# Kernel optimization log

Measured on AMD Instinct MI355X. Metric: run time of the kernel, lower is better.

The kernel has to match this reference:

```python
import jax, jax.numpy as jnp
import numpy as np

B, T, H = 4, 8192, 512
LN_EPS = 1e-5


def _ln(x, g, b):
    mu = jnp.mean(x, axis=-1, keepdims=True)
    var = jnp.mean((x - mu) ** 2, axis=-1, keepdims=True)
    return (x - mu) * jax.lax.rsqrt(var + LN_EPS) * g + b


def _log_g(x):
    # log of g(x) = x + 0.5 (x >= 0) else sigmoid(x); both branches NaN-safe.
    return jnp.where(x >= 0, jnp.log(jax.nn.relu(x) + 0.5), -jax.nn.softplus(-x))


def _min_gru(x, Wz, bz, Wh, bh):
    # minGRU parallel log-space scan ("Were RNNs All We Needed?" Alg.), h_0 = 0.
    k = x @ Wz + bz                      # [B,T,H] gate pre-activation
    log_z = -jax.nn.softplus(-k)         # log sigmoid(k)
    log_coeffs = -jax.nn.softplus(k)     # log (1 - sigmoid(k))
    log_tilde_h = _log_g(x @ Wh + bh)
    log_h0 = jnp.full((x.shape[0], 1, x.shape[2]), jnp.log(0.5), x.dtype)  # g(0)=0.5
    log_values = jnp.concatenate([log_h0, log_z + log_tilde_h], axis=1)   # [B,T+1,H]
    a_star = jnp.cumsum(jnp.pad(log_coeffs, ((0, 0), (1, 0), (0, 0))), axis=1)
    log_h = a_star + jax.lax.cumlogsumexp(log_values - a_star, axis=1)
    return jnp.exp(log_h)[:, 1:]         # drop h_0 slot -> [B,T,H]


def setup_inputs() -> dict:
    key = jax.random.key(0)
    ks = jax.random.split(key, 5)
    s = 1.0 / np.sqrt(H)
    return {
        "x": jax.random.normal(ks[0], (B, T, H), jnp.float32),
        "ln1_g": jnp.ones((H,), jnp.float32),
        "ln1_b": jnp.zeros((H,), jnp.float32),
        "Wz": jax.random.normal(ks[1], (H, H), jnp.float32) * s,
        "bz": jnp.zeros((H,), jnp.float32),
        "Wh": jax.random.normal(ks[2], (H, H), jnp.float32) * s,
        "bh": jnp.zeros((H,), jnp.float32),
        "ln2_g": jnp.ones((H,), jnp.float32),
        "ln2_b": jnp.zeros((H,), jnp.float32),
        "W1": jax.random.normal(ks[3], (H, H), jnp.float32) * s,
        "b1": jnp.zeros((H,), jnp.float32),
        "W2": jax.random.normal(ks[4], (H, H), jnp.float32) * s,
        "b2": jnp.zeros((H,), jnp.float32),
    }


def reference(x, ln1_g, ln1_b, Wz, bz, Wh, bh, ln2_g, ln2_b, W1, b1, W2, b2):
    # x = x + minGRU(ln_1(x))   (dropout=0 -> identity)
    x = x + _min_gru(_ln(x, ln1_g, ln1_b), Wz, bz, Wh, bh)
    # x = x + FFN(ln_2(x)) ; FFN = Linear -> ReLU -> Linear (hidden->hidden)
    h = jax.nn.relu(_ln(x, ln2_g, ln2_b) @ W1 + b1)
    x = x + (h @ W2 + b2)
    return x
```

## Files before the change

kernel.cpp:

```cpp
#include <hip/hip_runtime.h>

typedef unsigned short u16;
typedef unsigned int u32;
typedef __bf16 bf16x8 __attribute__((ext_vector_type(8)));
typedef float f32x4 __attribute__((ext_vector_type(4)));
typedef u16 u16x8 __attribute__((ext_vector_type(8)));

__device__ __forceinline__ u16 f2bf(float f) {
    union { float f; u32 i; } v; v.f = f;
    u32 x = v.i;
    u32 r = (x + 0x7fffu + ((x >> 16) & 1u)) >> 16;
    return (u16)r;
}
__device__ __forceinline__ float bf2f(u16 u) {
    union { u32 i; float f; } v; v.i = ((u32)u) << 16; return v.f;
}
__device__ __forceinline__ u16 f2h(float f) {
    union { _Float16 h; u16 u; } v; v.h = (_Float16)f; return v.u;
}
__device__ __forceinline__ float h2f(u16 u) {
    union { _Float16 h; u16 u; } v; v.u = u; return (float)v.h;
}

__device__ __forceinline__ void gld16(const void* g, void* l) {
    __builtin_amdgcn_global_load_lds(
        (const __attribute__((address_space(1))) void*)g,
        (__attribute__((address_space(3))) void*)l, 16, 0, 0);
}

__global__ __launch_bounds__(256) void transpose4(
    const float* __restrict__ s0, const float* __restrict__ s1,
    const float* __restrict__ s2, const float* __restrict__ s3,
    u16* __restrict__ d0, u16* __restrict__ d1,
    u16* __restrict__ d2, u16* __restrict__ d3)
{
    int bx = blockIdx.x;
    int mat = bx >> 8;
    int tile = bx & 255;
    int tx = (tile & 15) * 32;
    int ty = (tile >> 4) * 32;
    const float* src = (mat == 0) ? s0 : (mat == 1) ? s1 : (mat == 2) ? s2 : s3;
    u16* dst = (mat == 0) ? d0 : (mat == 1) ? d1 : (mat == 2) ? d2 : d3;

    __shared__ u16 tl[32][33];
    int col = threadIdx.x & 31;
    int r8  = threadIdx.x >> 5;
    #pragma unroll
    for (int k = 0; k < 4; ++k) {
        int rr = r8 + k * 8;
        tl[rr][col] = f2bf(src[(ty + rr) * 512 + tx + col]);
    }
    __syncthreads();
    #pragma unroll
    for (int k = 0; k < 4; ++k) {
        int rr = r8 + k * 8;
        dst[(tx + rr) * 512 + ty + col] = tl[col][rr];
    }
}

__global__ __launch_bounds__(256) void ln_k(
    const float* __restrict__ x, const float* __restrict__ g,
    const float* __restrict__ b, u16* __restrict__ y, int rows)
{
    int gid = blockIdx.x * blockDim.x + threadIdx.x;
    int row = gid >> 6;
    int lane = gid & 63;
    if (row >= rows) return;

    const float* xr = x + (size_t)row * 512 + lane * 8;
    float4 a0 = *(const float4*)xr;
    float4 a1 = *(const float4*)(xr + 4);
    float f[8] = {a0.x, a0.y, a0.z, a0.w, a1.x, a1.y, a1.z, a1.w};
    float s = 0.f, s2 = 0.f;
    #pragma unroll
    for (int e = 0; e < 8; ++e) { s += f[e]; s2 += f[e] * f[e]; }
    #pragma unroll
    for (int o = 32; o > 0; o >>= 1) { s += __shfl_xor(s, o); s2 += __shfl_xor(s2, o); }
    const float inv = 1.0f / 512.0f;
    float mean = s * inv;
    float var  = s2 * inv - mean * mean;
    float rstd = rsqrtf(var + 1e-5f);

    float4 g0 = *(const float4*)(g + lane * 8);
    float4 g1 = *(const float4*)(g + lane * 8 + 4);
    float4 b0 = *(const float4*)(b + lane * 8);
    float4 b1 = *(const float4*)(b + lane * 8 + 4);
    float gg[8] = {g0.x, g0.y, g0.z, g0.w, g1.x, g1.y, g1.z, g1.w};
    float bb[8] = {b0.x, b0.y, b0.z, b0.w, b1.x, b1.y, b1.z, b1.w};
    u16x8 ov;
    #pragma unroll
    for (int e = 0; e < 8; ++e)
        ov[e] = f2bf((f[e] - mean) * rstd * gg[e] + bb[e]);
    *(u16x8*)(y + (size_t)row * 512 + lane * 8) = ov;
}

__global__ __launch_bounds__(256, 2) void gemm_gate(
    const u16* __restrict__ A, const u16* __restrict__ Bt0,
    const u16* __restrict__ Bt1, const float* __restrict__ bias0,
    const float* __restrict__ bias1, u32* __restrict__ cvb,
    float* __restrict__ chCp, float* __restrict__ chVp)
{
    constexpr int Kd = 512, Nd = 512;
    constexpr int BUF = 12288;
    __shared__ __align__(16) u16 smem[2 * BUF];

    int bx = blockIdx.x;
    bx = (bx & 7) * 128 + (bx >> 3);
    int m0 = (bx >> 2) * 128;
    int n0 = (bx & 3) * 128;
    int tid = threadIdx.x;
    int lane = tid & 63;
    int w = tid >> 6;
    int wm = w & 1, wn = w >> 1;
    int l16 = lane & 15;
    int quad = lane >> 4;

    f32x4 acc0[4][4] = {};
    f32x4 acc1[4][4] = {};

    int ch0 = tid, ch1 = tid + 256;
    int row0 = ch0 >> 2, row1 = ch1 >> 2;
    int g0 = (ch0 & 3) ^ ((ch0 >> 3) & 3);
    int g1 = (ch1 & 3) ^ ((ch1 >> 3) & 3);
    const u16* a0p  = A   + (size_t)(m0 + row0) * Kd + g0 * 8;
    const u16* a1p  = A   + (size_t)(m0 + row1) * Kd + g1 * 8;
    const u16* b00p = Bt0 + (size_t)(n0 + row0) * Kd + g0 * 8;
    const u16* b01p = Bt0 + (size_t)(n0 + row1) * Kd + g1 * 8;
    const u16* b10p = Bt1 + (size_t)(n0 + row0) * Kd + g0 * 8;
    const u16* b11p = Bt1 + (size_t)(n0 + row1) * Kd + g1 * 8;

#define STAGE(sl, kt) { \
    int k0_ = (kt) * 32; \
    u16* L_ = smem + (sl) * BUF; \
    gld16(a0p  + k0_, &L_[ch0 * 8]); \
    gld16(a1p  + k0_, &L_[ch1 * 8]); \
    gld16(b00p + k0_, &L_[4096 + ch0 * 8]); \
    gld16(b01p + k0_, &L_[4096 + ch1 * 8]); \
    gld16(b10p + k0_, &L_[8192 + ch0 * 8]); \
    gld16(b11p + k0_, &L_[8192 + ch1 * 8]); }

    STAGE(0, 0);
    __syncthreads();

    for (int kt = 0; kt < Kd / 32; ++kt) {
        int cur = kt & 1;
        if (kt < Kd / 32 - 1) STAGE(cur ^ 1, kt + 1);

        const u16* As  = smem + cur * BUF;
        const u16* Bs0 = As + 4096;
        const u16* Bs1 = As + 8192;
        bf16x8 af[4], bf0[4], bf1[4];
        #pragma unroll
        for (int i = 0; i < 4; ++i) {
            int ra = wm * 64 + i * 16 + l16;
            int rb = wn * 64 + i * 16 + l16;
            int ga = quad ^ ((ra >> 1) & 3);
            int gb = quad ^ ((rb >> 1) & 3);
            af[i]  = *(const bf16x8*)&As [ra * 32 + ga * 8];
            bf0[i] = *(const bf16x8*)&Bs0[rb * 32 + gb * 8];
            bf1[i] = *(const bf16x8*)&Bs1[rb * 32 + gb * 8];
        }
        #pragma unroll
        for (int i = 0; i < 4; ++i)
            #pragma unroll
            for (int j = 0; j < 4; ++j) {
                acc0[i][j] = __builtin_amdgcn_mfma_f32_16x16x32_bf16(af[i], bf0[j], acc0[i][j], 0, 0, 0);
                acc1[i][j] = __builtin_amdgcn_mfma_f32_16x16x32_bf16(af[i], bf1[j], acc1[i][j], 0, 0, 0);
            }
        __syncthreads();
    }
#undef STAGE

    #pragma unroll
    for (int p = 0; p < 2; ++p) {
        int grow = m0 + wm * 64 + p * 32;
        int bb_  = grow >> 13;
        int chgl = (grow & 8191) >> 5;
        #pragma unroll
        for (int j = 0; j < 4; ++j) {
            int col = n0 + wn * 64 + j * 16 + l16;
            float bk  = bias0[col];
            float bh2 = bias1[col];
            float Cs[2], Vs[2];
            #pragma unroll
            for (int ii = 0; ii < 2; ++ii) {
                int i = 2 * p + ii;
                float C = 1.f, V = 0.f;
                #pragma unroll
                for (int r = 0; r < 4; ++r) {
                    int row = m0 + wm * 64 + i * 16 + quad * 4 + r;
                    float kk = acc0[i][j][r] + bk;
                    float hh = acc1[i][j][r] + bh2;
                    float z = __builtin_amdgcn_rcpf(1.f + __expf(-kk));
                    float c = 1.f - z;
                    float gs = __builtin_amdgcn_rcpf(1.f + __expf(-hh));
                    float gg = (hh >= 0.f) ? (hh + 0.5f) : gs;
                    float v = z * gg;
                    cvb[(size_t)row * Nd + col] =
                        (u32)f2h(c) | ((u32)f2h(v) << 16);
                    C *= c;
                    V = fmaf(c, V, v);
                }
                Cs[ii] = C; Vs[ii] = V;
            }
            #pragma unroll
            for (int ii = 0; ii < 2; ++ii) {
                float C = Cs[ii], V = Vs[ii];
                float oc = __shfl_xor(C, 16), ov = __shfl_xor(V, 16);
                V = (quad & 1) ? fmaf(C, ov, V) : fmaf(oc, V, ov);
                C *= oc;
                oc = __shfl_xor(C, 32); ov = __shfl_xor(V, 32);
                V = (quad & 2) ? fmaf(C, ov, V) : fmaf(oc, V, ov);
                C *= oc;
                Cs[ii] = C; Vs[ii] = V;
            }
            float Cch = Cs[0] * Cs[1];
            float Vch = fmaf(Cs[1], Vs[0], Vs[1]);
            if (quad == 0) {
                int idx = chgl * 2048 + bb_ * 512 + col;
                chCp[idx] = Cch;
                chVp[idx] = Vch;
            }
        }
    }
}

template <int EPI>
__global__ __launch_bounds__(256, 2) void gemm_wide(
    const u16* __restrict__ A, const u16* __restrict__ Bt,
    const float* __restrict__ bias, const float* __restrict__ resid,
    void* __restrict__ outv)
{
    constexpr int Kd = 512, Nd = 512;
    constexpr int BUF = 12288;
    __shared__ __align__(16) u16 smem[2 * BUF];

    int bx = blockIdx.x;
    bx = (bx & 7) * 64 + (bx >> 3);
    int m0 = (bx >> 2) * 256;
    int n0 = (bx & 3) * 128;
    int tid = threadIdx.x;
    int lane = tid & 63;
    int w = tid >> 6;
    int l16 = lane & 15;
    int quad = lane >> 4;

    f32x4 acc[4][8] = {};

    const u16* aP[4];
    const u16* bP[2];
    #pragma unroll
    for (int q = 0; q < 4; ++q) {
        int ch = tid + q * 256;
        int row = ch >> 2;
        int g = (ch & 3) ^ ((ch >> 3) & 3);
        aP[q] = A + (size_t)(m0 + row) * Kd + g * 8;
    }
    #pragma unroll
    for (int q = 0; q < 2; ++q) {
        int ch = tid + q * 256;
        int row = ch >> 2;
        int g = (ch & 3) ^ ((ch >> 3) & 3);
        bP[q] = Bt + (size_t)(n0 + row) * Kd + g * 8;
    }

#define STAGE(sl, kt) { \
    int k0_ = (kt) * 32; \
    u16* L_ = smem + (sl) * BUF; \
    gld16(aP[0] + k0_, &L_[(tid) * 8]); \
    gld16(aP[1] + k0_, &L_[(tid + 256) * 8]); \
    gld16(aP[2] + k0_, &L_[(tid + 512) * 8]); \
    gld16(aP[3] + k0_, &L_[(tid + 768) * 8]); \
    gld16(bP[0] + k0_, &L_[8192 + (tid) * 8]); \
    gld16(bP[1] + k0_, &L_[8192 + (tid + 256) * 8]); }

    STAGE(0, 0);
    __syncthreads();

    for (int kt = 0; kt < Kd / 32; ++kt) {
        int cur = kt & 1;
        if (kt < Kd / 32 - 1) STAGE(cur ^ 1, kt + 1);

        const u16* As = smem + cur * BUF;
        const u16* Bs = As + 8192;
        bf16x8 af[4], bf[8];
        #pragma unroll
        for (int i = 0; i < 4; ++i) {
            int ra = w * 64 + i * 16 + l16;
            int ga = quad ^ ((ra >> 1) & 3);
            af[i] = *(const bf16x8*)&As[ra * 32 + ga * 8];
        }
        #pragma unroll
        for (int j = 0; j < 8; ++j) {
            int rb = j * 16 + l16;
            int gb = quad ^ ((rb >> 1) & 3);
            bf[j] = *(const bf16x8*)&Bs[rb * 32 + gb * 8];
        }
        #pragma unroll
        for (int i = 0; i < 4; ++i)
            #pragma unroll
            for (int j = 0; j < 8; ++j)
                acc[i][j] = __builtin_amdgcn_mfma_f32_16x16x32_bf16(af[i], bf[j], acc[i][j], 0, 0, 0);
        __syncthreads();
    }
#undef STAGE

    #pragma unroll
    for (int j = 0; j < 8; ++j) {
        int col = n0 + j * 16 + l16;
        float bv = bias[col];
        #pragma unroll
        for (int i = 0; i < 4; ++i) {
            #pragma unroll
            for (int r = 0; r < 4; ++r) {
                int row = m0 + w * 64 + i * 16 + quad * 4 + r;
                size_t off = (size_t)row * Nd + col;
                float v = acc[i][j][r] + bv;
                if (EPI == 1) {
                    ((u16*)outv)[off] = f2bf(fmaxf(v, 0.f));
                } else {
                    ((float*)outv)[off] = v + resid[off];
                }
            }
        }
    }
}


__global__ __launch_bounds__(256) void scanB1(
    const float* __restrict__ chC, const float* __restrict__ chV,
    float* __restrict__ scC, float* __restrict__ scV)
{
    int gid = blockIdx.x * 256 + threadIdx.x;
    int s = gid & 2047;
    int sc = gid >> 11;
    float C = 1.f, V = 0.f;
    #pragma unroll 4
    for (int i = 0; i < 16; ++i) {
        int ch = sc * 16 + i;
        float c = chC[ch * 2048 + s];
        float v = chV[ch * 2048 + s];
        C *= c;
        V = fmaf(c, V, v);
    }
    scC[sc * 2048 + s] = C;
    scV[sc * 2048 + s] = V;
}

__global__ __launch_bounds__(256) void scanB2(
    const float* __restrict__ scC, const float* __restrict__ scV,
    float* __restrict__ sst)
{
    int s = blockIdx.x * 256 + threadIdx.x;
    float hcur = 0.5f;
    #pragma unroll
    for (int sc = 0; sc < 16; ++sc) {
        sst[sc * 2048 + s] = hcur;
        hcur = fmaf(scC[sc * 2048 + s], hcur, scV[sc * 2048 + s]);
    }
}

__global__ __launch_bounds__(256) void scanB3(
    const float* __restrict__ chC, const float* __restrict__ chV,
    const float* __restrict__ sst, float* __restrict__ hst)
{
    int gid = blockIdx.x * 256 + threadIdx.x;
    int s = gid & 2047;
    int sc = gid >> 11;
    float hcur = sst[sc * 2048 + s];
    #pragma unroll 4
    for (int i = 0; i < 16; ++i) {
        int ch = sc * 16 + i;
        hst[ch * 2048 + s] = hcur;
        hcur = fmaf(chC[ch * 2048 + s], hcur, chV[ch * 2048 + s]);
    }
}

__global__ __launch_bounds__(256) void scanC(
    const u32* __restrict__ cv, const float* __restrict__ hst,
    const float* __restrict__ x, float* __restrict__ x2)
{
    int gid = blockIdx.x * 256 + threadIdx.x;
    int h2 = (gid & 255) * 2;
    int rest = gid >> 8;
    int b = rest & 3;
    int ch = rest >> 2;
    size_t base = ((size_t)(b * 8192 + ch * 32)) * 512 + h2;
    int sidx = ch * 2048 + b * 512 + h2;
    float h0 = hst[sidx], h1 = hst[sidx + 1];
    #pragma unroll 8
    for (int t = 0; t < 32; ++t) {
        size_t off = base + (size_t)t * 512;
        uint2 g2 = *(const uint2*)(cv + off);
        float2 xx = *(const float2*)(x + off);
        h0 = fmaf(h2f((u16)(g2.x & 0xffffu)), h0, h2f((u16)(g2.x >> 16)));
        h1 = fmaf(h2f((u16)(g2.y & 0xffffu)), h1, h2f((u16)(g2.y >> 16)));
        float2 o; o.x = xx.x + h0; o.y = xx.y + h1;
        *(float2*)(x2 + off) = o;
    }
}

extern "C" void kernel_launch(void* const* d_in, const int* in_sizes, int n_in,
                              void* d_out, int out_size, void* d_ws, size_t ws_size,
                              hipStream_t stream)
{
    const float* x    = (const float*)d_in[0];
    const float* ln1g = (const float*)d_in[1];
    const float* ln1b = (const float*)d_in[2];
    const float* Wz   = (const float*)d_in[3];
    const float* bz   = (const float*)d_in[4];
    const float* Wh   = (const float*)d_in[5];
    const float* bh   = (const float*)d_in[6];
    const float* ln2g = (const float*)d_in[7];
    const float* ln2b = (const float*)d_in[8];
    const float* W1   = (const float*)d_in[9];
    const float* b1   = (const float*)d_in[10];
    const float* W2   = (const float*)d_in[11];
    const float* b2   = (const float*)d_in[12];
    float* out = (float*)d_out;

    char* ws = (char*)d_ws;
    constexpr size_t MB = 1024 * 1024;
    u16* Wzt = (u16*)(ws);
    u16* Wht = Wzt + 262144;
    u16* W1t = Wzt + 524288;
    u16* W2t = Wzt + 786432;
    u16* a   = (u16*)(ws + 3 * MB + 512 * 1024);
    u32* cv  = (u32*)(ws + 35 * MB + 512 * 1024);
    u16* hid = (u16*)(ws + 35 * MB + 512 * 1024);
    float* hst = (float*)(ws + 3 * MB + 512 * 1024);
    float* scC = hst + 524288;
    float* scV = scC + 32768;
    float* sst = scV + 32768;
    float* chC = (float*)d_out;
    float* chV = chC + 524288;

    transpose4<<<1024, 256, 0, stream>>>(Wz, Wh, W1, W2, Wzt, Wht, W1t, W2t);
    ln_k<<<8192, 256, 0, stream>>>(x, ln1g, ln1b, a, 32768);
    gemm_gate<<<1024, 256, 0, stream>>>(a, Wzt, Wht, bz, bh, cv, chC, chV);
    scanB1<<<128, 256, 0, stream>>>(chC, chV, scC, scV);
    scanB2<<<8, 256, 0, stream>>>(scC, scV, sst);
    scanB3<<<128, 256, 0, stream>>>(chC, chV, sst, hst);
    scanC<<<1024, 256, 0, stream>>>(cv, hst, x, out);
    ln_k<<<8192, 256, 0, stream>>>(out, ln2g, ln2b, a, 32768);
    gemm_wide<1><<<512, 256, 0, stream>>>(a, W1t, b1, nullptr, hid);
    gemm_wide<2><<<512, 256, 0, stream>>>(hid, W2t, b2, out, out);
}
```

Before: 301.2 us.

## Fuse prep kernels, collapse three-pass scan, and retile FFN GEMMs to 128x128

Merges the weight transpose and first LayerNorm into one launch. It replaces the three-kernel chunk-state scan with a single kernel in which each block recomputes the prefix over the preceding chunks. The FFN GEMMs move from 256x128 tiles to 128x128 tiles with a 2x2 warp layout and more blocks, and the launch-bounds occupancy hints rise. Fewer launches and better occupancy are the aim, traded against redundant prefix work in the scan (up to 240 serial chunk steps for the last blocks) and less data reuse per tile.

```diff
diff --git a/kernel.cpp b/kernel.cpp
--- a/kernel.cpp
+++ b/kernel.cpp
@@ -28,57 +28,54 @@
         (__attribute__((address_space(3))) void*)l, 16, 0, 0);
 }
 
-__global__ __launch_bounds__(256) void transpose4(
-    const float* __restrict__ s0, const float* __restrict__ s1,
-    const float* __restrict__ s2, const float* __restrict__ s3,
+__global__ __launch_bounds__(256) void prep(
+    const float* __restrict__ x, const float* __restrict__ g,
+    const float* __restrict__ b, u16* __restrict__ y,
+    const float* __restrict__ w0, const float* __restrict__ w1,
+    const float* __restrict__ w2, const float* __restrict__ w3,
     u16* __restrict__ d0, u16* __restrict__ d1,
     u16* __restrict__ d2, u16* __restrict__ d3)
 {
-    int bx = blockIdx.x;
-    int mat = bx >> 8;
-    int tile = bx & 255;
-    int tx = (tile & 15) * 32;
-    int ty = (tile >> 4) * 32;
-    const float* src = (mat == 0) ? s0 : (mat == 1) ? s1 : (mat == 2) ? s2 : s3;
-    u16* dst = (mat == 0) ? d0 : (mat == 1) ? d1 : (mat == 2) ? d2 : d3;
-
     __shared__ u16 tl[32][33];
-    int col = threadIdx.x & 31;
-    int r8  = threadIdx.x >> 5;
-    #pragma unroll
-    for (int k = 0; k < 4; ++k) {
-        int rr = r8 + k * 8;
-        tl[rr][col] = f2bf(src[(ty + rr) * 512 + tx + col]);
-    }
-    __syncthreads();
-    #pragma unroll
-    for (int k = 0; k < 4; ++k) {
-        int rr = r8 + k * 8;
-        dst[(tx + rr) * 512 + ty + col] = tl[col][rr];
-    }
-}
-
-__global__ __launch_bounds__(256) void ln_k(
-    const float* __restrict__ x, const float* __restrict__ g,
-    const float* __restrict__ b, u16* __restrict__ y, int rows)
-{
-    int gid = blockIdx.x * blockDim.x + threadIdx.x;
+    if (blockIdx.x < 1024) {
+        int bx = blockIdx.x;
+        int mat = bx >> 8;
+        int tile = bx & 255;
+        int tx = (tile & 15) * 32;
+        int ty = (tile >> 4) * 32;
+        const float* src = (mat == 0) ? w0 : (mat == 1) ? w1 : (mat == 2) ? w2 : w3;
+        u16* dst = (mat == 0) ? d0 : (mat == 1) ? d1 : (mat == 2) ? d2 : d3;
+        int col = threadIdx.x & 31;
+        int r8  = threadIdx.x >> 5;
+        #pragma unroll
+        for (int k = 0; k < 4; ++k) {
+            int rr = r8 + k * 8;
+            tl[rr][col] = f2bf(src[(ty + rr) * 512 + tx + col]);
+        }
+        __syncthreads();
+        #pragma unroll
+        for (int k = 0; k < 4; ++k) {
+            int rr = r8 + k * 8;
+            dst[(tx + rr) * 512 + ty + col] = tl[col][rr];
+        }
+        return;
+    }
+    int gid = (blockIdx.x - 1024) * 256 + threadIdx.x;
     int row = gid >> 6;
     int lane = gid & 63;
-    if (row >= rows) return;
 
     const float* xr = x + (size_t)row * 512 + lane * 8;
     float4 a0 = *(const float4*)xr;
     float4 a1 = *(const float4*)(xr + 4);
     float f[8] = {a0.x, a0.y, a0.z, a0.w, a1.x, a1.y, a1.z, a1.w};
-    float s = 0.f, s2 = 0.f;
-    #pragma unroll
-    for (int e = 0; e < 8; ++e) { s += f[e]; s2 += f[e] * f[e]; }
-    #pragma unroll
-    for (int o = 32; o > 0; o >>= 1) { s += __shfl_xor(s, o); s2 += __shfl_xor(s2, o); }
+    float sm = 0.f, sm2 = 0.f;
+    #pragma unroll
+    for (int e = 0; e < 8; ++e) { sm += f[e]; sm2 += f[e] * f[e]; }
+    #pragma unroll
+    for (int o = 32; o > 0; o >>= 1) { sm += __shfl_xor(sm, o); sm2 += __shfl_xor(sm2, o); }
     const float inv = 1.0f / 512.0f;
-    float mean = s * inv;
-    float var  = s2 * inv - mean * mean;
+    float mean = sm * inv;
+    float var  = sm2 * inv - mean * mean;
     float rstd = rsqrtf(var + 1e-5f);
 
     float4 g0 = *(const float4*)(g + lane * 8);
@@ -94,7 +91,43 @@
     *(u16x8*)(y + (size_t)row * 512 + lane * 8) = ov;
 }
 
-__global__ __launch_bounds__(256, 2) void gemm_gate(
+__global__ __launch_bounds__(256) void ln_k(
+    const float* __restrict__ x, const float* __restrict__ g,
+    const float* __restrict__ b, u16* __restrict__ y, int rows)
+{
+    int gid = blockIdx.x * blockDim.x + threadIdx.x;
+    int row = gid >> 6;
+    int lane = gid & 63;
+    if (row >= rows) return;
+
+    const float* xr = x + (size_t)row * 512 + lane * 8;
+    float4 a0 = *(const float4*)xr;
+    float4 a1 = *(const float4*)(xr + 4);
+    float f[8] = {a0.x, a0.y, a0.z, a0.w, a1.x, a1.y, a1.z, a1.w};
+    float sm = 0.f, sm2 = 0.f;
+    #pragma unroll
+    for (int e = 0; e < 8; ++e) { sm += f[e]; sm2 += f[e] * f[e]; }
+    #pragma unroll
+    for (int o = 32; o > 0; o >>= 1) { sm += __shfl_xor(sm, o); sm2 += __shfl_xor(sm2, o); }
+    const float inv = 1.0f / 512.0f;
+    float mean = sm * inv;
+    float var  = sm2 * inv - mean * mean;
+    float rstd = rsqrtf(var + 1e-5f);
+
+    float4 g0 = *(const float4*)(g + lane * 8);
+    float4 g1 = *(const float4*)(g + lane * 8 + 4);
+    float4 b0 = *(const float4*)(b + lane * 8);
+    float4 b1 = *(const float4*)(b + lane * 8 + 4);
+    float gg[8] = {g0.x, g0.y, g0.z, g0.w, g1.x, g1.y, g1.z, g1.w};
+    float bb[8] = {b0.x, b0.y, b0.z, b0.w, b1.x, b1.y, b1.z, b1.w};
+    u16x8 ov;
+    #pragma unroll
+    for (int e = 0; e < 8; ++e)
+        ov[e] = f2bf((f[e] - mean) * rstd * gg[e] + bb[e]);
+    *(u16x8*)(y + (size_t)row * 512 + lane * 8) = ov;
+}
+
+__global__ __launch_bounds__(256, 3) void gemm_gate(
     const u16* __restrict__ A, const u16* __restrict__ Bt0,
     const u16* __restrict__ Bt1, const float* __restrict__ bias0,
     const float* __restrict__ bias1, u32* __restrict__ cvb,
@@ -225,54 +258,45 @@
     }
 }
 
-template <int EPI>
-__global__ __launch_bounds__(256, 2) void gemm_wide(
-    const u16* __restrict__ A, const u16* __restrict__ Bt,
-    const float* __restrict__ bias, const float* __restrict__ resid,
-    void* __restrict__ outv)
+template <int MODE>
+__global__ __launch_bounds__(256, 4) void gemm_bt(
+    const u16* __restrict__ A, const u16* __restrict__ Bt0,
+    const float* __restrict__ bias0, const float* __restrict__ resid,
+    void* __restrict__ out0v)
 {
     constexpr int Kd = 512, Nd = 512;
-    constexpr int BUF = 12288;
+    constexpr int BUF = 8192;
     __shared__ __align__(16) u16 smem[2 * BUF];
 
     int bx = blockIdx.x;
-    bx = (bx & 7) * 64 + (bx >> 3);
-    int m0 = (bx >> 2) * 256;
+    bx = (bx & 7) * 128 + (bx >> 3);
+    int m0 = (bx >> 2) * 128;
     int n0 = (bx & 3) * 128;
     int tid = threadIdx.x;
     int lane = tid & 63;
     int w = tid >> 6;
+    int wm = w & 1, wn = w >> 1;
     int l16 = lane & 15;
     int quad = lane >> 4;
 
-    f32x4 acc[4][8] = {};
-
-    const u16* aP[4];
-    const u16* bP[2];
-    #pragma unroll
-    for (int q = 0; q < 4; ++q) {
-        int ch = tid + q * 256;
-        int row = ch >> 2;
-        int g = (ch & 3) ^ ((ch >> 3) & 3);
-        aP[q] = A + (size_t)(m0 + row) * Kd + g * 8;
-    }
-    #pragma unroll
-    for (int q = 0; q < 2; ++q) {
-        int ch = tid + q * 256;
-        int row = ch >> 2;
-        int g = (ch & 3) ^ ((ch >> 3) & 3);
-        bP[q] = Bt + (size_t)(n0 + row) * Kd + g * 8;
-    }
+    f32x4 acc0[4][4] = {};
+
+    int ch0 = tid, ch1 = tid + 256;
+    int row0 = ch0 >> 2, row1 = ch1 >> 2;
+    int g0 = (ch0 & 3) ^ ((ch0 >> 3) & 3);
+    int g1 = (ch1 & 3) ^ ((ch1 >> 3) & 3);
+    const u16* a0p  = A   + (size_t)(m0 + row0) * Kd + g0 * 8;
+    const u16* a1p  = A   + (size_t)(m0 + row1) * Kd + g1 * 8;
+    const u16* b00p = Bt0 + (size_t)(n0 + row0) * Kd + g0 * 8;
+    const u16* b01p = Bt0 + (size_t)(n0 + row1) * Kd + g1 * 8;
 
 #define STAGE(sl, kt) { \
     int k0_ = (kt) * 32; \
     u16* L_ = smem + (sl) * BUF; \
-    gld16(aP[0] + k0_, &L_[(tid) * 8]); \
-    gld16(aP[1] + k0_, &L_[(tid + 256) * 8]); \
-    gld16(aP[2] + k0_, &L_[(tid + 512) * 8]); \
-    gld16(aP[3] + k0_, &L_[(tid + 768) * 8]); \
-    gld16(bP[0] + k0_, &L_[8192 + (tid) * 8]); \
-    gld16(bP[1] + k0_, &L_[8192 + (tid + 256) * 8]); }
+    gld16(a0p  + k0_, &L_[ch0 * 8]); \
+    gld16(a1p  + k0_, &L_[ch1 * 8]); \
+    gld16(b00p + k0_, &L_[4096 + ch0 * 8]); \
+    gld16(b01p + k0_, &L_[4096 + ch1 * 8]); }
 
     STAGE(0, 0);
     __syncthreads();
@@ -281,98 +305,65 @@
         int cur = kt & 1;
         if (kt < Kd / 32 - 1) STAGE(cur ^ 1, kt + 1);
 
-        const u16* As = smem + cur * BUF;
-        const u16* Bs = As + 8192;
-        bf16x8 af[4], bf[8];
+        const u16* As  = smem + cur * BUF;
+        const u16* Bs0 = As + 4096;
+        bf16x8 af[4], bf0[4];
         #pragma unroll
         for (int i = 0; i < 4; ++i) {
-            int ra = w * 64 + i * 16 + l16;
+            int ra = wm * 64 + i * 16 + l16;
+            int rb = wn * 64 + i * 16 + l16;
             int ga = quad ^ ((ra >> 1) & 3);
-            af[i] = *(const bf16x8*)&As[ra * 32 + ga * 8];
-        }
-        #pragma unroll
-        for (int j = 0; j < 8; ++j) {
-            int rb = j * 16 + l16;
             int gb = quad ^ ((rb >> 1) & 3);
-            bf[j] = *(const bf16x8*)&Bs[rb * 32 + gb * 8];
+            af[i]  = *(const bf16x8*)&As [ra * 32 + ga * 8];
+            bf0[i] = *(const bf16x8*)&Bs0[rb * 32 + gb * 8];
         }
         #pragma unroll
         for (int i = 0; i < 4; ++i)
             #pragma unroll
-            for (int j = 0; j < 8; ++j)
-                acc[i][j] = __builtin_amdgcn_mfma_f32_16x16x32_bf16(af[i], bf[j], acc[i][j], 0, 0, 0);
+            for (int j = 0; j < 4; ++j)
+                acc0[i][j] = __builtin_amdgcn_mfma_f32_16x16x32_bf16(af[i], bf0[j], acc0[i][j], 0, 0, 0);
         __syncthreads();
     }
 #undef STAGE
 
     #pragma unroll
-    for (int j = 0; j < 8; ++j) {
-        int col = n0 + j * 16 + l16;
-        float bv = bias[col];
+    for (int j = 0; j < 4; ++j) {
+        int col = n0 + wn * 64 + j * 16 + l16;
+        float b0 = bias0[col];
         #pragma unroll
         for (int i = 0; i < 4; ++i) {
             #pragma unroll
             for (int r = 0; r < 4; ++r) {
-                int row = m0 + w * 64 + i * 16 + quad * 4 + r;
+                int row = m0 + wm * 64 + i * 16 + quad * 4 + r;
                 size_t off = (size_t)row * Nd + col;
-                float v = acc[i][j][r] + bv;
-                if (EPI == 1) {
-                    ((u16*)outv)[off] = f2bf(fmaxf(v, 0.f));
+                float v0 = acc0[i][j][r] + b0;
+                if (MODE == 1) {
+                    ((u16*)out0v)[off] = f2bf(fmaxf(v0, 0.f));
                 } else {
-                    ((float*)outv)[off] = v + resid[off];
+                    ((float*)out0v)[off] = v0 + resid[off];
                 }
             }
         }
     }
 }
 
-
-__global__ __launch_bounds__(256) void scanB1(
+__global__ __launch_bounds__(256) void scanB(
     const float* __restrict__ chC, const float* __restrict__ chV,
-    float* __restrict__ scC, float* __restrict__ scV)
-{
-    int gid = blockIdx.x * 256 + threadIdx.x;
-    int s = gid & 2047;
-    int sc = gid >> 11;
-    float C = 1.f, V = 0.f;
-    #pragma unroll 4
+    float* __restrict__ hst)
+{
+    int bx = blockIdx.x;
+    int sc = bx >> 3;
+    int s  = (bx & 7) * 256 + threadIdx.x;
+    float h = 0.5f;
+    int pre = sc * 16;
+    #pragma unroll 8
+    for (int c = 0; c < pre; ++c)
+        h = fmaf(chC[c * 2048 + s], h, chV[c * 2048 + s]);
+    #pragma unroll
     for (int i = 0; i < 16; ++i) {
         int ch = sc * 16 + i;
-        float c = chC[ch * 2048 + s];
-        float v = chV[ch * 2048 + s];
-        C *= c;
-        V = fmaf(c, V, v);
-    }
-    scC[sc * 2048 + s] = C;
-    scV[sc * 2048 + s] = V;
-}
-
-__global__ __launch_bounds__(256) void scanB2(
-    const float* __restrict__ scC, const float* __restrict__ scV,
-    float* __restrict__ sst)
-{
-    int s = blockIdx.x * 256 + threadIdx.x;
-    float hcur = 0.5f;
-    #pragma unroll
-    for (int sc = 0; sc < 16; ++sc) {
-        sst[sc * 2048 + s] = hcur;
-        hcur = fmaf(scC[sc * 2048 + s], hcur, scV[sc * 2048 + s]);
-    }
-}
-
-__global__ __launch_bounds__(256) void scanB3(
-    const float* __restrict__ chC, const float* __restrict__ chV,
-    const float* __restrict__ sst, float* __restrict__ hst)
-{
-    int gid = blockIdx.x * 256 + threadIdx.x;
-    int s = gid & 2047;
-    int sc = gid >> 11;
-    float hcur = sst[sc * 2048 + s];
-    #pragma unroll 4
-    for (int i = 0; i < 16; ++i) {
-        int ch = sc * 16 + i;
-        hst[ch * 2048 + s] = hcur;
-        hcur = fmaf(chC[ch * 2048 + s], hcur, chV[ch * 2048 + s]);
+        hst[ch * 2048 + s] = h;
+        h = fmaf(chC[ch * 2048 + s], h, chV[ch * 2048 + s]);
     }
 }
 
@@ -429,20 +420,15 @@
     u32* cv  = (u32*)(ws + 35 * MB + 512 * 1024);
     u16* hid = (u16*)(ws + 35 * MB + 512 * 1024);
     float* hst = (float*)(ws + 3 * MB + 512 * 1024);
-    float* scC = hst + 524288;
-    float* scV = scC + 32768;
-    float* sst = scV + 32768;
     float* chC = (float*)d_out;
     float* chV = chC + 524288;
 
-    transpose4<<<1024, 256, 0, stream>>>(Wz, Wh, W1, W2, Wzt, Wht, W1t, W2t);
-    ln_k<<<8192, 256, 0, stream>>>(x, ln1g, ln1b, a, 32768);
+    prep<<<9216, 256, 0, stream>>>(x, ln1g, ln1b, a,
+                                   Wz, Wh, W1, W2, Wzt, Wht, W1t, W2t);
     gemm_gate<<<1024, 256, 0, stream>>>(a, Wzt, Wht, bz, bh, cv, chC, chV);
-    scanB1<<<128, 256, 0, stream>>>(chC, chV, scC, scV);
-    scanB2<<<8, 256, 0, stream>>>(scC, scV, sst);
-    scanB3<<<128, 256, 0, stream>>>(chC, chV, sst, hst);
+    scanB<<<128, 256, 0, stream>>>(chC, chV, hst);
     scanC<<<1024, 256, 0, stream>>>(cv, hst, x, out);
     ln_k<<<8192, 256, 0, stream>>>(out, ln2g, ln2b, a, 32768);
-    gemm_wide<1><<<512, 256, 0, stream>>>(a, W1t, b1, nullptr, hid);
-    gemm_wide<2><<<512, 256, 0, stream>>>(hid, W2t, b2, out, out);
-}
+    gemm_bt<1><<<1024, 256, 0, stream>>>(a, W1t, b1, nullptr, hid);
+    gemm_bt<2><<<1024, 256, 0, stream>>>(hid, W2t, b2, out, out);
+}
```

Result: slower. 342.2 us (+13.6%).
